# Kernel tuning notes

Measured on AMD Instinct MI355X. Metric: run time of the kernel, lower is better.

The kernel has to match this reference:

```python
import jax, jax.numpy as jnp
import numpy as np

N, C, F = 16384, 8, 257
EPS = 1e-6
DELTA_MAX = 1e8


def setup_inputs() -> dict:
    key = jax.random.key(0)
    k1, k2, k3 = jax.random.split(key, 3)
    xr = jax.random.normal(k1, (N, C, F), dtype=jnp.float32)
    xi = jax.random.normal(k2, (N, C, F), dtype=jnp.float32)
    # affine params (reset_parameters: Wrr=Wii=1, Wri~U(-0.9,0.9), Br=Bi=0)
    Wrr = jnp.ones((C, F), dtype=jnp.float32)
    Wri = jax.random.uniform(k3, (C, F), dtype=jnp.float32, minval=-0.9, maxval=0.9)
    Wii = jnp.ones((C, F), dtype=jnp.float32)
    Br = jnp.zeros((C, F), dtype=jnp.float32)
    Bi = jnp.zeros((C, F), dtype=jnp.float32)
    return {"xr": xr, "xi": xi, "Wrr": Wrr, "Wri": Wri, "Wii": Wii, "Br": Br, "Bi": Bi}


def reference(xr, xi, Wrr, Wri, Wii, Br, Bi):
    # batch (training-mode) complex batchnorm over dim 0; stats per (channel, feature)
    Mr = jnp.mean(xr, axis=0, keepdims=True)  # [1,C,F]
    Mi = jnp.mean(xi, axis=0, keepdims=True)
    xr = xr - Mr
    xi = xi - Mi
    Vrr = jnp.mean(xr * xr, axis=0, keepdims=True)  # [1,C,F]
    Vri = jnp.mean(xr * xi, axis=0, keepdims=True)
    Vii = jnp.mean(xi * xi, axis=0, keepdims=True)
    tau = Vrr + Vii
    delta = jnp.clip(Vrr * Vii - Vri * Vri, EPS, DELTA_MAX)
    s = jnp.sqrt(delta)
    t = jnp.sqrt(tau + 2.0 * s)
    rst = 1.0 / (s * t)
    # inverse matrix square root of 2x2 covariance
    Urr = (s + Vii) * rst
    Uii = (s + Vrr) * rst
    Uri = -Vri * rst
    # affine mixing: Z = W @ U  (W, B broadcast [C,F] against [1,C,F])
    Zrr = Wrr * Urr + Wri * Uri
    Zri = Wrr * Uri + Wri * Uii
    Zir = Wri * Urr + Wii * Uri
    Zii = Wri * Uri + Wii * Uii
    yr = Zrr * xr + Zri * xi + Br
    yi = Zir * xr + Zii * xi + Bi
    return (yr, yi)
```

## Files before the change

kernel.cpp:

```cpp
#include <hip/hip_runtime.h>
#include <stdint.h>

#define NROWS   16384
#define NCOLS   2056
#define NG      257
#define NQ      514
#define EPSV    1e-6f
#define DELTA_MAX 1e8f
#define NSUM    (5*NCOLS)
#define T8TOT   (NROWS*NG)
#define T4TOT   (NROWS*NQ)

typedef float    f32x4 __attribute__((ext_vector_type(4)));
typedef uint32_t u32x4 __attribute__((ext_vector_type(4)));

__device__ __forceinline__ float bf_lo(uint32_t u) {
    return __builtin_bit_cast(float, u << 16);
}
__device__ __forceinline__ float bf_hi(uint32_t u) {
    return __builtin_bit_cast(float, u & 0xffff0000u);
}
__device__ __forceinline__ float bf1(uint16_t u) {
    return __builtin_bit_cast(float, (uint32_t)u << 16);
}
__device__ __forceinline__ uint32_t bf16pair(float lo, float hi) {
    uint32_t ul = __builtin_bit_cast(uint32_t, lo);
    uint32_t uh = __builtin_bit_cast(uint32_t, hi);
    ul = (ul + 0x7fffu + ((ul >> 16) & 1u)) >> 16;
    uh = (uh + 0x7fffu + ((uh >> 16) & 1u)) & 0xffff0000u;
    return ul | uh;
}

__global__ __launch_bounds__(512) void detect_kernel(
    const uint32_t* __restrict__ xr_u, const uint32_t* __restrict__ wrr_u,
    int* __restrict__ flags)
{
    __shared__ int cnt[2];
    if (threadIdx.x < 2) cnt[threadIdx.x] = 0;
    __syncthreads();
    const int part = threadIdx.x >> 8;
    const uint32_t u = part ? wrr_u[threadIdx.x & 255] : xr_u[threadIdx.x & 255];
    const uint32_t e = (u >> 7) & 0xFFu;
    const int ok = (e >= 100u && e <= 131u) ? 1 : 0;
    atomicAdd(&cnt[part], ok);
    __syncthreads();
    if (threadIdx.x == 0) {
        flags[0] = (cnt[0] < 128) ? 1 : 0;
        flags[1] = (cnt[1] < 128) ? 1 : 0;
    }
}

__global__ __launch_bounds__(1024, 8) void stats_kernel(
    const void* __restrict__ xr_p, const void* __restrict__ xi_p,
    const int* __restrict__ flags, float* __restrict__ partials,
    int TT, int nit8, int nit4)
{
    __shared__ float lds[NSUM];
    const int t = threadIdx.x;
    for (int i = t; i < NSUM; i += 1024) lds[i] = 0.f;
    const int tid = blockIdx.x * 1024 + t;

    if (!flags[0]) {
        float acc[40];
        #pragma unroll
        for (int j = 0; j < 40; ++j) acc[j] = 0.f;
        const uint4* __restrict__ xr4 = (const uint4*)xr_p;
        const uint4* __restrict__ xi4 = (const uint4*)xi_p;
        for (int k = 0; k < nit8; ++k) {
            const size_t g = (size_t)tid + (size_t)k * TT;
            const uint4 a = xr4[g];
            const uint4 b = xi4[g];
            const uint32_t au[4] = {a.x, a.y, a.z, a.w};
            const uint32_t bu[4] = {b.x, b.y, b.z, b.w};
            #pragma unroll
            for (int j = 0; j < 4; ++j) {
                const float r0 = bf_lo(au[j]), r1 = bf_hi(au[j]);
                const float i0 = bf_lo(bu[j]), i1 = bf_hi(bu[j]);
                acc[0*8 + 2*j]     += r0;       acc[1*8 + 2*j]     += i0;
                acc[2*8 + 2*j]     += r0*r0;    acc[3*8 + 2*j]     += r0*i0;
                acc[4*8 + 2*j]     += i0*i0;
                acc[0*8 + 2*j + 1] += r1;       acc[1*8 + 2*j + 1] += i1;
                acc[2*8 + 2*j + 1] += r1*r1;    acc[3*8 + 2*j + 1] += r1*i1;
                acc[4*8 + 2*j + 1] += i1*i1;
            }
        }
        __syncthreads();
        const int c  = tid % NG;
        const int ph = t / NG;
        for (int p = 0; p < 4; ++p) {
            if (ph == p) {
                #pragma unroll
                for (int s = 0; s < 5; ++s)
                    #pragma unroll
                    for (int j = 0; j < 8; ++j)
                        lds[s*NCOLS + c*8 + j] += acc[s*8 + j];
            }
            __syncthreads();
        }
    } else {
        float acc[20];
        #pragma unroll
        for (int j = 0; j < 20; ++j) acc[j] = 0.f;
        const float4* __restrict__ xr4 = (const float4*)xr_p;
        const float4* __restrict__ xi4 = (const float4*)xi_p;
        for (int k = 0; k < nit4; ++k) {
            const size_t g = (size_t)tid + (size_t)k * TT;
            const float4 a = xr4[g];
            const float4 b = xi4[g];
            const float xr[4] = {a.x, a.y, a.z, a.w};
            const float xi[4] = {b.x, b.y, b.z, b.w};
            #pragma unroll
            for (int j = 0; j < 4; ++j) {
                acc[0*4 + j] += xr[j];        acc[1*4 + j] += xi[j];
                acc[2*4 + j] += xr[j]*xr[j];  acc[3*4 + j] += xr[j]*xi[j];
                acc[4*4 + j] += xi[j]*xi[j];
            }
        }
        __syncthreads();
        const int cq = tid % NQ;
        const int ph = t / NQ;
        for (int p = 0; p < 2; ++p) {
            if (ph == p) {
                #pragma unroll
                for (int s = 0; s < 5; ++s)
                    #pragma unroll
                    for (int j = 0; j < 4; ++j)
                        lds[s*NCOLS + cq*4 + j] += acc[s*4 + j];
            }
            __syncthreads();
        }
    }

    float* __restrict__ dst = partials + (size_t)blockIdx.x * NSUM;
    for (int i = t; i < NSUM; i += 1024)
        __builtin_nontemporal_store(lds[i], dst + i);
}

__global__ __launch_bounds__(256) void reduce_kernel(
    const float* __restrict__ partials, float* __restrict__ sums, int NB)
{
    const int j  = blockIdx.x * 64 + (threadIdx.x & 63);
    const int bl = threadIdx.x >> 6;
    float s = 0.f;
    if (j < NSUM) {
        #pragma unroll 4
        for (int b = bl; b < NB; b += 4)
            s += partials[(size_t)b * NSUM + j];
    }
    __shared__ float red[256];
    red[threadIdx.x] = s;
    __syncthreads();
    if (threadIdx.x < 64 && j < NSUM)
        sums[j] = red[threadIdx.x] + red[threadIdx.x + 64] +
                  red[threadIdx.x + 128] + red[threadIdx.x + 192];
}

__global__ __launch_bounds__(256) void coef_kernel(
    const float* __restrict__ sums,
    const void* __restrict__ Wrr_p, const void* __restrict__ Wri_p,
    const void* __restrict__ Wii_p, const void* __restrict__ Br_p,
    const void* __restrict__ Bi_p,
    const int* __restrict__ flags, float* __restrict__ coef)
{
    const int j = blockIdx.x * 256 + threadIdx.x;
    if (j >= NCOLS) return;
    const float invN = 1.0f / (float)NROWS;
    const float Mr  = sums[0*NCOLS+j] * invN;
    const float Mi  = sums[1*NCOLS+j] * invN;
    const float Vrr = sums[2*NCOLS+j] * invN - Mr * Mr;
    const float Vri = sums[3*NCOLS+j] * invN - Mr * Mi;
    const float Vii = sums[4*NCOLS+j] * invN - Mi * Mi;
    const float tau   = Vrr + Vii;
    const float delta = fminf(fmaxf(Vrr * Vii - Vri * Vri, EPSV), DELTA_MAX);
    const float s   = sqrtf(delta);
    const float t   = sqrtf(tau + 2.0f * s);
    const float rst = 1.0f / (s * t);
    const float Urr = (s + Vii) * rst;
    const float Uii = (s + Vrr) * rst;
    const float Uri = -Vri * rst;

    float wrr, wri, wii, br, bi;
    if (flags[1]) {
        wrr = ((const float*)Wrr_p)[j];  wri = ((const float*)Wri_p)[j];
        wii = ((const float*)Wii_p)[j];
        br  = ((const float*)Br_p)[j];   bi  = ((const float*)Bi_p)[j];
    } else {
        wrr = bf1(((const uint16_t*)Wrr_p)[j]);  wri = bf1(((const uint16_t*)Wri_p)[j]);
        wii = bf1(((const uint16_t*)Wii_p)[j]);
        br  = bf1(((const uint16_t*)Br_p)[j]);   bi  = bf1(((const uint16_t*)Bi_p)[j]);
    }
    const float Zrr = wrr * Urr + wri * Uri;
    const float Zri = wrr * Uri + wri * Uii;
    const float Zir = wri * Urr + wii * Uri;
    const float Zii = wri * Uri + wii * Uii;
    coef[0*NCOLS+j] = Zrr;
    coef[1*NCOLS+j] = Zri;
    coef[2*NCOLS+j] = Zir;
    coef[3*NCOLS+j] = Zii;
    coef[4*NCOLS+j] = br - Zrr * Mr - Zri * Mi;
    coef[5*NCOLS+j] = bi - Zir * Mr - Zii * Mi;
}

__global__ __launch_bounds__(256) void apply_kernel(
    const void* __restrict__ xr_p, const void* __restrict__ xi_p,
    const float* __restrict__ coef, const int* __restrict__ flags,
    void* __restrict__ out_p)
{
    const int tid = blockIdx.x * 256 + threadIdx.x;
    const int c  = tid % NG;
    const int r0 = tid / NG;
    const int col = c * 8;

    float Z[6][8];
    #pragma unroll
    for (int t = 0; t < 6; ++t) {
        const float4 lo = *(const float4*)(coef + t*NCOLS + col);
        const float4 hi = *(const float4*)(coef + t*NCOLS + col + 4);
        Z[t][0]=lo.x; Z[t][1]=lo.y; Z[t][2]=lo.z; Z[t][3]=lo.w;
        Z[t][4]=hi.x; Z[t][5]=hi.y; Z[t][6]=hi.z; Z[t][7]=hi.w;
    }

    if (flags[0]) {
        const float4* xr4 = (const float4*)xr_p;
        const float4* xi4 = (const float4*)xi_p;
        f32x4* yr4 = (f32x4*)out_p;
        f32x4* yi4 = yr4 + (size_t)NROWS * NQ;
        #pragma unroll 2
        for (int k = 0; k < 8; ++k) {
            const size_t g = (size_t)(r0 + (k << 11)) * NQ + 2 * c;
            const float4 a0 = xr4[g], a1 = xr4[g + 1];
            const float4 b0 = xi4[g], b1 = xi4[g + 1];
            const float xrv[8] = {a0.x,a0.y,a0.z,a0.w,a1.x,a1.y,a1.z,a1.w};
            const float xiv[8] = {b0.x,b0.y,b0.z,b0.w,b1.x,b1.y,b1.z,b1.w};
            float yrv[8], yiv[8];
            #pragma unroll
            for (int j = 0; j < 8; ++j) {
                yrv[j] = Z[0][j]*xrv[j] + Z[1][j]*xiv[j] + Z[4][j];
                yiv[j] = Z[2][j]*xrv[j] + Z[3][j]*xiv[j] + Z[5][j];
            }
            const f32x4 s0 = {yrv[0], yrv[1], yrv[2], yrv[3]};
            const f32x4 s1 = {yrv[4], yrv[5], yrv[6], yrv[7]};
            const f32x4 t0 = {yiv[0], yiv[1], yiv[2], yiv[3]};
            const f32x4 t1 = {yiv[4], yiv[5], yiv[6], yiv[7]};
            __builtin_nontemporal_store(s0, yr4 + g);
            __builtin_nontemporal_store(s1, yr4 + g + 1);
            __builtin_nontemporal_store(t0, yi4 + g);
            __builtin_nontemporal_store(t1, yi4 + g + 1);
        }
    } else {
        const uint4* xr4 = (const uint4*)xr_p;
        const uint4* xi4 = (const uint4*)xi_p;
        u32x4* yr4 = (u32x4*)out_p;
        u32x4* yi4 = yr4 + (size_t)NROWS * NG;
        #pragma unroll 2
        for (int k = 0; k < 8; ++k) {
            const size_t g = (size_t)(r0 + (k << 11)) * NG + c;
            const uint4 a = xr4[g];
            const uint4 b = xi4[g];
            const uint32_t au[4] = {a.x, a.y, a.z, a.w};
            const uint32_t bu[4] = {b.x, b.y, b.z, b.w};
            uint32_t ou[4], pu[4];
            #pragma unroll
            for (int j = 0; j < 4; ++j) {
                const int e0 = 2*j, e1 = 2*j + 1;
                const float xr0 = bf_lo(au[j]), xr1 = bf_hi(au[j]);
                const float xi0 = bf_lo(bu[j]), xi1 = bf_hi(bu[j]);
                const float yr0 = Z[0][e0]*xr0 + Z[1][e0]*xi0 + Z[4][e0];
                const float yi0 = Z[2][e0]*xr0 + Z[3][e0]*xi0 + Z[5][e0];
                const float yr1 = Z[0][e1]*xr1 + Z[1][e1]*xi1 + Z[4][e1];
                const float yi1 = Z[2][e1]*xr1 + Z[3][e1]*xi1 + Z[5][e1];
                ou[j] = bf16pair(yr0, yr1);
                pu[j] = bf16pair(yi0, yi1);
            }
            const u32x4 o = {ou[0], ou[1], ou[2], ou[3]};
            const u32x4 p = {pu[0], pu[1], pu[2], pu[3]};
            __builtin_nontemporal_store(o, yr4 + g);
            __builtin_nontemporal_store(p, yi4 + g);
        }
    }
}

extern "C" void kernel_launch(void* const* d_in, const int* in_sizes, int n_in,
                              void* d_out, int out_size, void* d_ws, size_t ws_size,
                              hipStream_t stream)
{
    const void* xr_p = d_in[0];
    const void* xi_p = d_in[1];
    const void* Wrr  = d_in[2];
    const void* Wri  = d_in[3];
    const void* Wii  = d_in[4];
    const void* Br   = d_in[5];
    const void* Bi   = d_in[6];

    float* sums  = (float*)d_ws;
    float* coef  = sums + NSUM;
    int*   flags = (int*)(coef + 6 * NCOLS);
    float* partials = (float*)(flags + 4);

    const size_t base_bytes = (size_t)(NSUM + 6 * NCOLS + 4) * 4;
    int NB = 514;
    if (base_bytes + (size_t)NB * NSUM * 4 > ws_size) NB = 257;
    const int TT   = NB * 1024;
    const int nit8 = T8TOT / TT;
    const int nit4 = T4TOT / TT;

    detect_kernel<<<1, 512, 0, stream>>>((const uint32_t*)xr_p, (const uint32_t*)Wrr, flags);
    stats_kernel<<<NB, 1024, 0, stream>>>(xr_p, xi_p, flags, partials, TT, nit8, nit4);
    reduce_kernel<<<(NSUM + 63) / 64, 256, 0, stream>>>(partials, sums, NB);
    coef_kernel<<<(NCOLS + 255) / 256, 256, 0, stream>>>(sums, Wrr, Wri, Wii, Br, Bi, flags, coef);
    apply_kernel<<<2056, 256, 0, stream>>>(xr_p, xi_p, coef, flags, d_out);
}
```

Measured before the change: 547.1 us.

## Shrink stats blocks, drop serialized LDS merge, fuse reduce with coef

The stats kernel now runs 256-thread blocks, so each thread owns distinct columns. Each thread writes its accumulators straight to LDS instead of going through a phased, barrier-serialized add. The separate reduce and coefficient kernels are merged into one launch that sums five statistics per column and then computes the whitening and affine coefficients. The apply kernel's math is rewritten with 8-wide vector types. The trade-off is a 4x smaller stats grid with more iterations per thread, which may lower the memory parallelism in flight.

Result: slower. 660.4 us (+20.7%).

```diff
diff --git a/kernel.cpp b/kernel.cpp
--- a/kernel.cpp
+++ b/kernel.cpp
@@ -11,8 +11,9 @@
 #define T8TOT   (NROWS*NG)
 #define T4TOT   (NROWS*NQ)
 
-typedef float    f32x4 __attribute__((ext_vector_type(4)));
-typedef uint32_t u32x4 __attribute__((ext_vector_type(4)));
+typedef float    f32x4v __attribute__((ext_vector_type(4)));
+typedef float    f32x8v __attribute__((ext_vector_type(8)));
+typedef uint32_t u32x4v __attribute__((ext_vector_type(4)));
 
 __device__ __forceinline__ float bf_lo(uint32_t u) {
     return __builtin_bit_cast(float, u << 16);
@@ -50,20 +51,20 @@
     }
 }
 
-__global__ __launch_bounds__(1024, 8) void stats_kernel(
+__global__ __launch_bounds__(256, 1) void stats_kernel(
     const void* __restrict__ xr_p, const void* __restrict__ xi_p,
     const int* __restrict__ flags, float* __restrict__ partials,
     int TT, int nit8, int nit4)
 {
     __shared__ float lds[NSUM];
     const int t = threadIdx.x;
-    for (int i = t; i < NSUM; i += 1024) lds[i] = 0.f;
-    const int tid = blockIdx.x * 1024 + t;
+    const int tid = blockIdx.x * 256 + t;
+    for (int i = t; i < NSUM; i += 256) lds[i] = 0.f;
+    __syncthreads();
 
     if (!flags[0]) {
-        float acc[40];
-        #pragma unroll
-        for (int j = 0; j < 40; ++j) acc[j] = 0.f;
+        f32x8v sr  = {0.f,0.f,0.f,0.f,0.f,0.f,0.f,0.f};
+        f32x8v si  = sr, srr = sr, sri = sr, sii = sr;
         const uint4* __restrict__ xr4 = (const uint4*)xr_p;
         const uint4* __restrict__ xi4 = (const uint4*)xi_p;
         for (int k = 0; k < nit8; ++k) {
@@ -76,31 +77,24 @@
             for (int j = 0; j < 4; ++j) {
                 const float r0 = bf_lo(au[j]), r1 = bf_hi(au[j]);
                 const float i0 = bf_lo(bu[j]), i1 = bf_hi(bu[j]);
-                acc[0*8 + 2*j]     += r0;       acc[1*8 + 2*j]     += i0;
-                acc[2*8 + 2*j]     += r0*r0;    acc[3*8 + 2*j]     += r0*i0;
-                acc[4*8 + 2*j]     += i0*i0;
-                acc[0*8 + 2*j + 1] += r1;       acc[1*8 + 2*j + 1] += i1;
-                acc[2*8 + 2*j + 1] += r1*r1;    acc[3*8 + 2*j + 1] += r1*i1;
-                acc[4*8 + 2*j + 1] += i1*i1;
-            }
-        }
-        __syncthreads();
-        const int c  = tid % NG;
-        const int ph = t / NG;
-        for (int p = 0; p < 4; ++p) {
-            if (ph == p) {
-                #pragma unroll
-                for (int s = 0; s < 5; ++s)
-                    #pragma unroll
-                    for (int j = 0; j < 8; ++j)
-                        lds[s*NCOLS + c*8 + j] += acc[s*8 + j];
-            }
-            __syncthreads();
+                sr [2*j]   += r0;       si [2*j]   += i0;
+                srr[2*j]   += r0*r0;    sri[2*j]   += r0*i0;    sii[2*j]   += i0*i0;
+                sr [2*j+1] += r1;       si [2*j+1] += i1;
+                srr[2*j+1] += r1*r1;    sri[2*j+1] += r1*i1;    sii[2*j+1] += i1*i1;
+            }
+        }
+        const int c = tid % NG;
+        #pragma unroll
+        for (int j = 0; j < 8; ++j) {
+            lds[0*NCOLS + c*8 + j] = sr [j];
+            lds[1*NCOLS + c*8 + j] = si [j];
+            lds[2*NCOLS + c*8 + j] = srr[j];
+            lds[3*NCOLS + c*8 + j] = sri[j];
+            lds[4*NCOLS + c*8 + j] = sii[j];
         }
     } else {
-        float acc[20];
-        #pragma unroll
-        for (int j = 0; j < 20; ++j) acc[j] = 0.f;
+        f32x4v sr  = {0.f,0.f,0.f,0.f};
+        f32x4v si  = sr, srr = sr, sri = sr, sii = sr;
         const float4* __restrict__ xr4 = (const float4*)xr_p;
         const float4* __restrict__ xi4 = (const float4*)xi_p;
         for (int k = 0; k < nit4; ++k) {
@@ -111,94 +105,93 @@
             const float xi[4] = {b.x, b.y, b.z, b.w};
             #pragma unroll
             for (int j = 0; j < 4; ++j) {
-                acc[0*4 + j] += xr[j];        acc[1*4 + j] += xi[j];
-                acc[2*4 + j] += xr[j]*xr[j];  acc[3*4 + j] += xr[j]*xi[j];
-                acc[4*4 + j] += xi[j]*xi[j];
-            }
-        }
-        __syncthreads();
+                sr [j] += xr[j];        si [j] += xi[j];
+                srr[j] += xr[j]*xr[j];  sri[j] += xr[j]*xi[j];  sii[j] += xi[j]*xi[j];
+            }
+        }
         const int cq = tid % NQ;
-        const int ph = t / NQ;
-        for (int p = 0; p < 2; ++p) {
-            if (ph == p) {
-                #pragma unroll
-                for (int s = 0; s < 5; ++s)
-                    #pragma unroll
-                    for (int j = 0; j < 4; ++j)
-                        lds[s*NCOLS + cq*4 + j] += acc[s*4 + j];
-            }
-            __syncthreads();
-        }
-    }
-
+        #pragma unroll
+        for (int j = 0; j < 4; ++j) {
+            lds[0*NCOLS + cq*4 + j] = sr [j];
+            lds[1*NCOLS + cq*4 + j] = si [j];
+            lds[2*NCOLS + cq*4 + j] = srr[j];
+            lds[3*NCOLS + cq*4 + j] = sri[j];
+            lds[4*NCOLS + cq*4 + j] = sii[j];
+        }
+    }
+
+    __syncthreads();
     float* __restrict__ dst = partials + (size_t)blockIdx.x * NSUM;
-    for (int i = t; i < NSUM; i += 1024)
+    for (int i = t; i < NSUM; i += 256)
         __builtin_nontemporal_store(lds[i], dst + i);
 }
 
-__global__ __launch_bounds__(256) void reduce_kernel(
-    const float* __restrict__ partials, float* __restrict__ sums, int NB)
-{
-    const int j  = blockIdx.x * 64 + (threadIdx.x & 63);
-    const int bl = threadIdx.x >> 6;
-    float s = 0.f;
-    if (j < NSUM) {
-        #pragma unroll 4
-        for (int b = bl; b < NB; b += 4)
-            s += partials[(size_t)b * NSUM + j];
-    }
-    __shared__ float red[256];
-    red[threadIdx.x] = s;
-    __syncthreads();
-    if (threadIdx.x < 64 && j < NSUM)
-        sums[j] = red[threadIdx.x] + red[threadIdx.x + 64] +
-                  red[threadIdx.x + 128] + red[threadIdx.x + 192];
-}
-
-__global__ __launch_bounds__(256) void coef_kernel(
-    const float* __restrict__ sums,
+__global__ __launch_bounds__(256) void reduce_coef_kernel(
+    const float* __restrict__ partials,
     const void* __restrict__ Wrr_p, const void* __restrict__ Wri_p,
     const void* __restrict__ Wii_p, const void* __restrict__ Br_p,
     const void* __restrict__ Bi_p,
-    const int* __restrict__ flags, float* __restrict__ coef)
-{
-    const int j = blockIdx.x * 256 + threadIdx.x;
-    if (j >= NCOLS) return;
-    const float invN = 1.0f / (float)NROWS;
-    const float Mr  = sums[0*NCOLS+j] * invN;
-    const float Mi  = sums[1*NCOLS+j] * invN;
-    const float Vrr = sums[2*NCOLS+j] * invN - Mr * Mr;
-    const float Vri = sums[3*NCOLS+j] * invN - Mr * Mi;
-    const float Vii = sums[4*NCOLS+j] * invN - Mi * Mi;
-    const float tau   = Vrr + Vii;
-    const float delta = fminf(fmaxf(Vrr * Vii - Vri * Vri, EPSV), DELTA_MAX);
-    const float s   = sqrtf(delta);
-    const float t   = sqrtf(tau + 2.0f * s);
-    const float rst = 1.0f / (s * t);
-    const float Urr = (s + Vii) * rst;
-    const float Uii = (s + Vrr) * rst;
-    const float Uri = -Vri * rst;
-
-    float wrr, wri, wii, br, bi;
-    if (flags[1]) {
-        wrr = ((const float*)Wrr_p)[j];  wri = ((const float*)Wri_p)[j];
-        wii = ((const float*)Wii_p)[j];
-        br  = ((const float*)Br_p)[j];   bi  = ((const float*)Bi_p)[j];
-    } else {
-        wrr = bf1(((const uint16_t*)Wrr_p)[j]);  wri = bf1(((const uint16_t*)Wri_p)[j]);
-        wii = bf1(((const uint16_t*)Wii_p)[j]);
-        br  = bf1(((const uint16_t*)Br_p)[j]);   bi  = bf1(((const uint16_t*)Bi_p)[j]);
-    }
-    const float Zrr = wrr * Urr + wri * Uri;
-    const float Zri = wrr * Uri + wri * Uii;
-    const float Zir = wri * Urr + wii * Uri;
-    const float Zii = wri * Uri + wii * Uii;
-    coef[0*NCOLS+j] = Zrr;
-    coef[1*NCOLS+j] = Zri;
-    coef[2*NCOLS+j] = Zir;
-    coef[3*NCOLS+j] = Zii;
-    coef[4*NCOLS+j] = br - Zrr * Mr - Zri * Mi;
-    coef[5*NCOLS+j] = bi - Zir * Mr - Zii * Mi;
+    const int* __restrict__ flags, float* __restrict__ coef, int NB)
+{
+    const int col = blockIdx.x * 64 + (threadIdx.x & 63);
+    const int bl  = threadIdx.x >> 6;
+    float a0 = 0.f, a1 = 0.f, a2 = 0.f, a3 = 0.f, a4 = 0.f;
+    if (col < NCOLS) {
+        for (int b = bl; b < NB; b += 4) {
+            const float* __restrict__ p = partials + (size_t)b * NSUM + col;
+            a0 += p[0*NCOLS]; a1 += p[1*NCOLS]; a2 += p[2*NCOLS];
+            a3 += p[3*NCOLS]; a4 += p[4*NCOLS];
+        }
+    }
+    __shared__ float red[5][256];
+    red[0][threadIdx.x] = a0; red[1][threadIdx.x] = a1; red[2][threadIdx.x] = a2;
+    red[3][threadIdx.x] = a3; red[4][threadIdx.x] = a4;
+    __syncthreads();
+    if (threadIdx.x < 64 && col < NCOLS) {
+        const int j = col;
+        const int u = threadIdx.x;
+        const float S0 = red[0][u] + red[0][u+64] + red[0][u+128] + red[0][u+192];
+        const float S1 = red[1][u] + red[1][u+64] + red[1][u+128] + red[1][u+192];
+        const float S2 = red[2][u] + red[2][u+64] + red[2][u+128] + red[2][u+192];
+        const float S3 = red[3][u] + red[3][u+64] + red[3][u+128] + red[3][u+192];
+        const float S4 = red[4][u] + red[4][u+64] + red[4][u+128] + red[4][u+192];
+
+        const float invN = 1.0f / (float)NROWS;
+        const float Mr  = S0 * invN;
+        const float Mi  = S1 * invN;
+        const float Vrr = S2 * invN - Mr * Mr;
+        const float Vri = S3 * invN - Mr * Mi;
+        const float Vii = S4 * invN - Mi * Mi;
+        const float tau   = Vrr + Vii;
+        const float delta = fminf(fmaxf(Vrr * Vii - Vri * Vri, EPSV), DELTA_MAX);
+        const float s   = sqrtf(delta);
+        const float t   = sqrtf(tau + 2.0f * s);
+        const float rst = 1.0f / (s * t);
+        const float Urr = (s + Vii) * rst;
+        const float Uii = (s + Vrr) * rst;
+        const float Uri = -Vri * rst;
+
+        float wrr, wri, wii, br, bi;
+        if (flags[1]) {
+            wrr = ((const float*)Wrr_p)[j];  wri = ((const float*)Wri_p)[j];
+            wii = ((const float*)Wii_p)[j];
+            br  = ((const float*)Br_p)[j];   bi  = ((const float*)Bi_p)[j];
+        } else {
+            wrr = bf1(((const uint16_t*)Wrr_p)[j]);  wri = bf1(((const uint16_t*)Wri_p)[j]);
+            wii = bf1(((const uint16_t*)Wii_p)[j]);
+            br  = bf1(((const uint16_t*)Br_p)[j]);   bi  = bf1(((const uint16_t*)Bi_p)[j]);
+        }
+        const float Zrr = wrr * Urr + wri * Uri;
+        const float Zri = wrr * Uri + wri * Uii;
+        const float Zir = wri * Urr + wii * Uri;
+        const float Zii = wri * Uri + wii * Uii;
+        coef[0*NCOLS+j] = Zrr;
+        coef[1*NCOLS+j] = Zri;
+        coef[2*NCOLS+j] = Zir;
+        coef[3*NCOLS+j] = Zii;
+        coef[4*NCOLS+j] = br - Zrr * Mr - Zri * Mi;
+        coef[5*NCOLS+j] = bi - Zir * Mr - Zii * Mi;
+    }
 }
 
 __global__ __launch_bounds__(256) void apply_kernel(
@@ -211,37 +204,34 @@
     const int r0 = tid / NG;
     const int col = c * 8;
 
-    float Z[6][8];
-    #pragma unroll
-    for (int t = 0; t < 6; ++t) {
-        const float4 lo = *(const float4*)(coef + t*NCOLS + col);
-        const float4 hi = *(const float4*)(coef + t*NCOLS + col + 4);
-        Z[t][0]=lo.x; Z[t][1]=lo.y; Z[t][2]=lo.z; Z[t][3]=lo.w;
-        Z[t][4]=hi.x; Z[t][5]=hi.y; Z[t][6]=hi.z; Z[t][7]=hi.w;
-    }
+    const f32x8v zrr = *(const f32x8v*)(coef + 0*NCOLS + col);
+    const f32x8v zri = *(const f32x8v*)(coef + 1*NCOLS + col);
+    const f32x8v zir = *(const f32x8v*)(coef + 2*NCOLS + col);
+    const f32x8v zii = *(const f32x8v*)(coef + 3*NCOLS + col);
+    const f32x8v cr  = *(const f32x8v*)(coef + 4*NCOLS + col);
+    const f32x8v ci  = *(const f32x8v*)(coef + 5*NCOLS + col);
 
     if (flags[0]) {
         const float4* xr4 = (const float4*)xr_p;
         const float4* xi4 = (const float4*)xi_p;
-        f32x4* yr4 = (f32x4*)out_p;
-        f32x4* yi4 = yr4 + (size_t)NROWS * NQ;
+        f32x4v* yr4 = (f32x4v*)out_p;
+        f32x4v* yi4 = yr4 + (size_t)NROWS * NQ;
         #pragma unroll 2
         for (int k = 0; k < 8; ++k) {
             const size_t g = (size_t)(r0 + (k << 11)) * NQ + 2 * c;
             const float4 a0 = xr4[g], a1 = xr4[g + 1];
             const float4 b0 = xi4[g], b1 = xi4[g + 1];
-            const float xrv[8] = {a0.x,a0.y,a0.z,a0.w,a1.x,a1.y,a1.z,a1.w};
-            const float xiv[8] = {b0.x,b0.y,b0.z,b0.w,b1.x,b1.y,b1.z,b1.w};
-            float yrv[8], yiv[8];
-            #pragma unroll
-            for (int j = 0; j < 8; ++j) {
-                yrv[j] = Z[0][j]*xrv[j] + Z[1][j]*xiv[j] + Z[4][j];
-                yiv[j] = Z[2][j]*xrv[j] + Z[3][j]*xiv[j] + Z[5][j];
-            }
-            const f32x4 s0 = {yrv[0], yrv[1], yrv[2], yrv[3]};
-            const f32x4 s1 = {yrv[4], yrv[5], yrv[6], yrv[7]};
-            const f32x4 t0 = {yiv[0], yiv[1], yiv[2], yiv[3]};
-            const f32x4 t1 = {yiv[4], yiv[5], yiv[6], yiv[7]};
+            f32x8v xv, yv;
+            xv[0]=a0.x; xv[1]=a0.y; xv[2]=a0.z; xv[3]=a0.w;
+            xv[4]=a1.x; xv[5]=a1.y; xv[6]=a1.z; xv[7]=a1.w;
+            yv[0]=b0.x; yv[1]=b0.y; yv[2]=b0.z; yv[3]=b0.w;
+            yv[4]=b1.x; yv[5]=b1.y; yv[6]=b1.z; yv[7]=b1.w;
+            const f32x8v yr = zrr*xv + zri*yv + cr;
+            const f32x8v yi = zir*xv + zii*yv + ci;
+            const f32x4v s0 = {yr[0], yr[1], yr[2], yr[3]};
+            const f32x4v s1 = {yr[4], yr[5], yr[6], yr[7]};
+            const f32x4v t0 = {yi[0], yi[1], yi[2], yi[3]};
+            const f32x4v t1 = {yi[4], yi[5], yi[6], yi[7]};
             __builtin_nontemporal_store(s0, yr4 + g);
             __builtin_nontemporal_store(s1, yr4 + g + 1);
             __builtin_nontemporal_store(t0, yi4 + g);
@@ -250,8 +240,8 @@
     } else {
         const uint4* xr4 = (const uint4*)xr_p;
         const uint4* xi4 = (const uint4*)xi_p;
-        u32x4* yr4 = (u32x4*)out_p;
-        u32x4* yi4 = yr4 + (size_t)NROWS * NG;
+        u32x4v* yr4 = (u32x4v*)out_p;
+        u32x4v* yi4 = yr4 + (size_t)NROWS * NG;
         #pragma unroll 2
         for (int k = 0; k < 8; ++k) {
             const size_t g = (size_t)(r0 + (k << 11)) * NG + c;
@@ -259,21 +249,20 @@
             const uint4 b = xi4[g];
             const uint32_t au[4] = {a.x, a.y, a.z, a.w};
             const uint32_t bu[4] = {b.x, b.y, b.z, b.w};
-            uint32_t ou[4], pu[4];
-            #pragma unroll
-            for (int j = 0; j < 4; ++j) {
-                const int e0 = 2*j, e1 = 2*j + 1;
-                const float xr0 = bf_lo(au[j]), xr1 = bf_hi(au[j]);
-                const float xi0 = bf_lo(bu[j]), xi1 = bf_hi(bu[j]);
-                const float yr0 = Z[0][e0]*xr0 + Z[1][e0]*xi0 + Z[4][e0];
-                const float yi0 = Z[2][e0]*xr0 + Z[3][e0]*xi0 + Z[5][e0];
-                const float yr1 = Z[0][e1]*xr1 + Z[1][e1]*xi1 + Z[4][e1];
-                const float yi1 = Z[2][e1]*xr1 + Z[3][e1]*xi1 + Z[5][e1];
-                ou[j] = bf16pair(yr0, yr1);
-                pu[j] = bf16pair(yi0, yi1);
-            }
-            const u32x4 o = {ou[0], ou[1], ou[2], ou[3]};
-            const u32x4 p = {pu[0], pu[1], pu[2], pu[3]};
+            f32x8v xv, yv;
+            #pragma unroll
+            for (int j = 0; j < 4; ++j) {
+                xv[2*j] = bf_lo(au[j]);  xv[2*j+1] = bf_hi(au[j]);
+                yv[2*j] = bf_lo(bu[j]);  yv[2*j+1] = bf_hi(bu[j]);
+            }
+            const f32x8v yr = zrr*xv + zri*yv + cr;
+            const f32x8v yi = zir*xv + zii*yv + ci;
+            u32x4v o, p;
+            #pragma unroll
+            for (int j = 0; j < 4; ++j) {
+                o[j] = bf16pair(yr[2*j], yr[2*j+1]);
+                p[j] = bf16pair(yi[2*j], yi[2*j+1]);
+            }
             __builtin_nontemporal_store(o, yr4 + g);
             __builtin_nontemporal_store(p, yi4 + g);
         }
@@ -292,21 +281,19 @@
     const void* Br   = d_in[5];
     const void* Bi   = d_in[6];
 
-    float* sums  = (float*)d_ws;
-    float* coef  = sums + NSUM;
+    float* coef  = (float*)d_ws;
     int*   flags = (int*)(coef + 6 * NCOLS);
-    float* partials = (float*)(flags + 4);
-
-    const size_t base_bytes = (size_t)(NSUM + 6 * NCOLS + 4) * 4;
+    float* partials = (float*)(flags + 16);
+
+    const size_t base_bytes = (size_t)(6 * NCOLS + 16) * 4;
     int NB = 514;
     if (base_bytes + (size_t)NB * NSUM * 4 > ws_size) NB = 257;
-    const int TT   = NB * 1024;
+    const int TT   = NB * 256;
     const int nit8 = T8TOT / TT;
     const int nit4 = T4TOT / TT;
 
     detect_kernel<<<1, 512, 0, stream>>>((const uint32_t*)xr_p, (const uint32_t*)Wrr, flags);
-    stats_kernel<<<NB, 1024, 0, stream>>>(xr_p, xi_p, flags, partials, TT, nit8, nit4);
-    reduce_kernel<<<(NSUM + 63) / 64, 256, 0, stream>>>(partials, sums, NB);
-    coef_kernel<<<(NCOLS + 255) / 256, 256, 0, stream>>>(sums, Wrr, Wri, Wii, Br, Bi, flags, coef);
+    stats_kernel<<<NB, 256, 0, stream>>>(xr_p, xi_p, flags, partials, TT, nit8, nit4);
+    reduce_coef_kernel<<<33, 256, 0, stream>>>(partials, Wrr, Wri, Wii, Br, Bi, flags, coef, NB);
     apply_kernel<<<2056, 256, 0, stream>>>(xr_p, xi_p, coef, flags, d_out);
 }
```
